# Kernel optimization log

Hardware: AMD Instinct MI355X
Metric: run time of the kernel (lower is better)

Reference implementation:

```python
import jax, jax.numpy as jnp
import numpy as np

# irreps "64x0e + 32x1o + 16x2e": dims 64*1 + 32*3 + 16*5 = 240
MUL = (64, 32, 16)
DEG = (1, 3, 5)  # 2l+1 for l=0,1,2
IRREPS_DIM = sum(m * d for m, d in zip(MUL, DEG))  # 240
N_NODES = 20000
N_EDGES = 320000


def equivariant_linear(x, W0, W1, W2):
    """e3nn-style linear: per-irrep channel mixing shared across m-components,
    with 1/sqrt(fan_in) path normalization."""
    ws = (W0, W1, W2)
    outs = []
    off = 0
    for (mul, deg, W) in zip(MUL, DEG, ws):
        blk = x[:, off:off + mul * deg].reshape(-1, mul, deg)  # (N, mul, 2l+1)
        y = jnp.einsum('oi,nid->nod', W, blk) / jnp.sqrt(jnp.asarray(mul, x.dtype))
        outs.append(y.reshape(-1, mul * deg))
        off += mul * deg
    return jnp.concatenate(outs, axis=-1)


def setup_inputs() -> dict:
    key = jax.random.key(0)
    k1, k2, k3, k4, k5, k6 = jax.random.split(key, 6)
    messages = jax.random.normal(k1, (N_EDGES, IRREPS_DIM), dtype=jnp.float32)
    edge_index = jax.random.randint(k2, (N_EDGES, 2), 0, N_NODES, dtype=jnp.int64)
    edge_cutoff = jax.random.uniform(k3, (N_EDGES,), dtype=jnp.float32)
    W0 = jax.random.normal(k4, (64, 64), dtype=jnp.float32)
    W1 = jax.random.normal(k5, (32, 32), dtype=jnp.float32)
    W2 = jax.random.normal(k6, (16, 16), dtype=jnp.float32)
    return {"messages": messages, "edge_index": edge_index, "edge_cutoff": edge_cutoff,
            "W0": W0, "W1": W1, "W2": W2, "n_nodes": N_NODES}


def reference(messages, edge_index, edge_cutoff, W0, W1, W2, n_nodes):
    target = edge_index[:, 1]
    weighted = messages * edge_cutoff[:, None]  # fused cutoff multiply
    agg = jax.ops.segment_sum(weighted, target, num_segments=n_nodes)  # (n_nodes, 240)
    return equivariant_linear(agg, W0, W1, W2)
```

## Files before the change

### kernel.cpp

```cpp
#include <hip/hip_runtime.h>

#define IRREPS 240

__global__ void histogram_kernel(const int* __restrict__ eidx, int* __restrict__ counts,
                                 int n_edges) {
    int e = blockIdx.x * blockDim.x + threadIdx.x;
    if (e >= n_edges) return;
    atomicAdd(&counts[eidx[2 * e + 1]], 1);
}

__global__ void scan_kernel(const int* __restrict__ counts, int* __restrict__ offsets,
                            int* __restrict__ cursor, int n) {
    __shared__ int part[1024];
    int t = threadIdx.x;
    int per = (n + 1023) / 1024;
    int start = t * per;
    int end = min(start + per, n);
    int sum = 0;
    for (int i = start; i < end; ++i) sum += counts[i];
    part[t] = sum;
    __syncthreads();
    for (int off = 1; off < 1024; off <<= 1) {
        int v = (t >= off) ? part[t - off] : 0;
        __syncthreads();
        part[t] += v;
        __syncthreads();
    }
    int run = (t == 0) ? 0 : part[t - 1];
    for (int i = start; i < end; ++i) {
        offsets[i] = run;
        cursor[i] = run;
        run += counts[i];
    }
}

__global__ void fill_kernel(const int* __restrict__ eidx, int* __restrict__ cursor,
                            int* __restrict__ edge_ids, int n_edges) {
    int e = blockIdx.x * blockDim.x + threadIdx.x;
    if (e >= n_edges) return;
    int tgt = eidx[2 * e + 1];
    int pos = atomicAdd(&cursor[tgt], 1);
    edge_ids[pos] = e;
}

__global__ void gather_linear_kernel(const float* __restrict__ msgs,
                                     const float* __restrict__ cutoff,
                                     const int* __restrict__ edge_ids,
                                     const int* __restrict__ offsets,
                                     const int* __restrict__ counts,
                                     const float* __restrict__ W0,
                                     const float* __restrict__ W1,
                                     const float* __restrict__ W2,
                                     float* __restrict__ out) {
    __shared__ float s[IRREPS];
    int n = blockIdx.x;
    int t = threadIdx.x;

    int beg = offsets[n];
    int cnt = counts[n];

    if (t < IRREPS) {
        float acc = 0.f;
        for (int j = beg; j < beg + cnt; ++j) {
            int e = edge_ids[j];
            float w = cutoff[e];
            acc += msgs[(long long)e * IRREPS + t] * w;
        }
        s[t] = acc;
    }
    __syncthreads();
    if (t >= IRREPS) return;

    float acc = 0.f;
    float res;
    if (t < 64) {
        int o = t;
        #pragma unroll 8
        for (int i = 0; i < 64; ++i) acc += W0[o * 64 + i] * s[i];
        res = acc * 0.125f;
    } else if (t < 160) {
        int rel = t - 64;
        int o = rel / 3, d = rel % 3;
        #pragma unroll 8
        for (int i = 0; i < 32; ++i) acc += W1[o * 32 + i] * s[64 + i * 3 + d];
        res = acc * 0.17677669529663687f;
    } else {
        int rel = t - 160;
        int o = rel / 5, d = rel % 5;
        #pragma unroll
        for (int i = 0; i < 16; ++i) acc += W2[o * 16 + i] * s[160 + i * 5 + d];
        res = acc * 0.25f;
    }
    out[(long long)n * IRREPS + t] = res;
}

extern "C" void kernel_launch(void* const* d_in, const int* in_sizes, int n_in,
                              void* d_out, int out_size, void* d_ws, size_t ws_size,
                              hipStream_t stream) {
    const float* msgs   = (const float*)d_in[0];
    const int*   eidx   = (const int*)d_in[1];
    const float* cutoff = (const float*)d_in[2];
    const float* W0     = (const float*)d_in[3];
    const float* W1     = (const float*)d_in[4];
    const float* W2     = (const float*)d_in[5];

    int n_edges = in_sizes[0] / IRREPS;
    int n_nodes = out_size / IRREPS;

    int* counts   = (int*)d_ws;
    int* offsets  = counts + n_nodes;
    int* cursor   = offsets + n_nodes;
    int* edge_ids = cursor + n_nodes;

    hipMemsetAsync(counts, 0, (size_t)n_nodes * sizeof(int), stream);

    int block = 256;
    int egrid = (n_edges + block - 1) / block;
    histogram_kernel<<<egrid, block, 0, stream>>>(eidx, counts, n_edges);
    scan_kernel<<<1, 1024, 0, stream>>>(counts, offsets, cursor, n_nodes);
    fill_kernel<<<egrid, block, 0, stream>>>(eidx, cursor, edge_ids, n_edges);
    gather_linear_kernel<<<n_nodes, 256, 0, stream>>>(
        msgs, cutoff, edge_ids, offsets, counts, W0, W1, W2, (float*)d_out);
}
```

Baseline: 216.1 us.

## Split gather across four wavefronts with float4 loads and staged edge ids

The per-node gather now stages batches of edge ids and cutoff weights in shared memory, then splits the edges across four 64-lane wavefronts. Each wavefront reads a message row with float4 loads, and the four partial sums are combined through shared memory. This replaces a serial per-thread loop of scalar loads with dependent index lookups, aiming for more memory-level parallelism and wider loads. It adds extra barriers and a shared-memory reduction. Four lanes per wavefront sit idle.

After: 178.5 us. 17.4% less time.

```diff
diff --git a/kernel.cpp b/kernel.cpp
--- a/kernel.cpp
+++ b/kernel.cpp
@@ -1,6 +1,7 @@
 #include <hip/hip_runtime.h>
 
 #define IRREPS 240
+#define BATCH 64
 
 __global__ void histogram_kernel(const int* __restrict__ eidx, int* __restrict__ counts,
                                  int n_edges) {
@@ -52,44 +53,74 @@
                                      const float* __restrict__ W1,
                                      const float* __restrict__ W2,
                                      float* __restrict__ out) {
+    __shared__ int   s_eid[BATCH];
+    __shared__ float s_w[BATCH];
+    __shared__ float s_part[4][IRREPS];
     __shared__ float s[IRREPS];
+
     int n = blockIdx.x;
     int t = threadIdx.x;
+    int es = t >> 6;
+    int lane = t & 63;
 
     int beg = offsets[n];
     int cnt = counts[n];
 
+    float4 acc = make_float4(0.f, 0.f, 0.f, 0.f);
+
+    for (int base = 0; base < cnt; base += BATCH) {
+        int bn = min(BATCH, cnt - base);
+        if (t < bn) {
+            int e = edge_ids[beg + base + t];
+            s_eid[t] = e;
+            s_w[t] = cutoff[e];
+        }
+        __syncthreads();
+        if (lane < 60) {
+            #pragma unroll 4
+            for (int i = es; i < bn; i += 4) {
+                int e = s_eid[i];
+                float w = s_w[i];
+                const float4 m = *reinterpret_cast<const float4*>(
+                    msgs + (long long)e * IRREPS + lane * 4);
+                acc.x += m.x * w;
+                acc.y += m.y * w;
+                acc.z += m.z * w;
+                acc.w += m.w * w;
+            }
+        }
+        __syncthreads();
+    }
+
+    if (lane < 60) {
+        *reinterpret_cast<float4*>(&s_part[es][lane * 4]) = acc;
+    }
+    __syncthreads();
     if (t < IRREPS) {
-        float acc = 0.f;
-        for (int j = beg; j < beg + cnt; ++j) {
-            int e = edge_ids[j];
-            float w = cutoff[e];
-            acc += msgs[(long long)e * IRREPS + t] * w;
-        }
-        s[t] = acc;
+        s[t] = s_part[0][t] + s_part[1][t] + s_part[2][t] + s_part[3][t];
     }
     __syncthreads();
     if (t >= IRREPS) return;
 
-    float acc = 0.f;
+    float a = 0.f;
     float res;
     if (t < 64) {
         int o = t;
         #pragma unroll 8
-        for (int i = 0; i < 64; ++i) acc += W0[o * 64 + i] * s[i];
-        res = acc * 0.125f;
+        for (int i = 0; i < 64; ++i) a += W0[o * 64 + i] * s[i];
+        res = a * 0.125f;
     } else if (t < 160) {
         int rel = t - 64;
         int o = rel / 3, d = rel % 3;
         #pragma unroll 8
-        for (int i = 0; i < 32; ++i) acc += W1[o * 32 + i] * s[64 + i * 3 + d];
-        res = acc * 0.17677669529663687f;
+        for (int i = 0; i < 32; ++i) a += W1[o * 32 + i] * s[64 + i * 3 + d];
+        res = a * 0.17677669529663687f;
     } else {
         int rel = t - 160;
         int o = rel / 5, d = rel % 5;
         #pragma unroll
-        for (int i = 0; i < 16; ++i) acc += W2[o * 16 + i] * s[160 + i * 5 + d];
-        res = acc * 0.25f;
+        for (int i = 0; i < 16; ++i) a += W2[o * 16 + i] * s[160 + i * 5 + d];
+        res = a * 0.25f;
     }
     out[(long long)n * IRREPS + t] = res;
 }
```
